# Kernel tuning notes

Hardware: AMD Instinct MI355X
Metric: run time of the kernel (lower is better)

The kernel has to match this reference:

```python
import jax, jax.numpy as jnp
import numpy as np

B, N, C = 128, 512, 512  # batch, num_proposals, hidden_dim
K = 3                    # kernel_size
EPS = 1e-5               # LayerNorm eps (torch default)


def setup_inputs() -> dict:
    key = jax.random.key(0)
    k1, k2, k3, k4 = jax.random.split(key, 4)
    query = jax.random.normal(k1, (B, N, C), dtype=jnp.float32)
    value = jax.random.normal(k2, (B, N, C), dtype=jnp.float32)
    # nn.Linear(C, N+K): store transposed weight [C, N+K] for x @ W
    lim = 1.0 / np.sqrt(C)
    W_lin = jax.random.uniform(k3, (C, N + K), minval=-lim, maxval=lim, dtype=jnp.float32)
    b_lin = jax.random.uniform(k4, (N + K,), minval=-lim, maxval=lim, dtype=jnp.float32)
    gamma = jnp.ones((C,), dtype=jnp.float32)
    beta = jnp.zeros((C,), dtype=jnp.float32)
    return {"query": query, "value": value, "W_lin": W_lin, "b_lin": b_lin,
            "gamma": gamma, "beta": beta}


def reference(query, value, W_lin, b_lin, gamma, beta):
    # dynamic weights: [B, N, N+K]
    dy = jnp.einsum('bnc,ck->bnk', query, W_lin) + b_lin
    dw = dy[..., :K]          # depthwise kernel  [B, N, 3]
    pw = dy[..., K:]          # pointwise weights [B, N(out), N(in)]
    # depthwise conv1d along C, groups=N, padding='same' (cross-correlation)
    vp = jnp.pad(value, ((0, 0), (0, 0), (1, 1)))
    depth = (dw[..., 0:1] * vp[..., 0:C]
             + dw[..., 1:2] * vp[..., 1:C + 1]
             + dw[..., 2:3] * vp[..., 2:C + 2])
    depth = jax.nn.relu(depth)
    # pointwise (1x1) conv across proposals: out[b,m,c] = sum_n pw[b,m,n] * depth[b,n,c]
    out = jnp.einsum('bmn,bnc->bmc', pw, depth)
    # LayerNorm over last dim C
    mu = jnp.mean(out, axis=-1, keepdims=True)
    var = jnp.mean(jnp.square(out - mu), axis=-1, keepdims=True)
    return (out - mu) * jax.lax.rsqrt(var + EPS) * gamma + beta
```

## Files before the change

kernel.cpp:

```cpp
#include <hip/hip_runtime.h>
#include <hip/hip_bf16.h>

typedef unsigned short u16;
typedef unsigned int u32;
typedef __attribute__((ext_vector_type(8))) short short8;
typedef __attribute__((ext_vector_type(8))) unsigned short ushort8;
typedef __attribute__((ext_vector_type(4))) float f32x4;

#define AS1 __attribute__((address_space(1)))
#define AS3 __attribute__((address_space(3)))

#define Bb_ 128
#define Nn_ 512
#define Cc_ 512
#define NK_ 515

__device__ __forceinline__ u16 f2bf(float f) {
    union { float f; u32 i; } t; t.f = f;
    u32 x = t.i;
    u32 r = (x + 0x7fffu + ((x >> 16) & 1u)) >> 16;
    return (u16)r;
}

#define ROWS_PER_WAVE 32
__global__ void prep_kernel(const float* __restrict__ q, const float* __restrict__ W,
                            const float* __restrict__ bl,
                            u16* __restrict__ qbf, float* __restrict__ dw) {
    __shared__ float wc[3][512];
    int tid = threadIdx.x;
    for (int idx = tid; idx < 3 * 512; idx += 256) {
        int j = idx >> 9, c = idx & 511;
        wc[j][c] = W[c * NK_ + j];
    }
    __syncthreads();

    int w = tid >> 6, l = tid & 63;
    int c0 = l * 8;
    float w0[8], w1[8], w2[8];
#pragma unroll
    for (int e = 0; e < 8; e++) {
        w0[e] = wc[0][c0 + e];
        w1[e] = wc[1][c0 + e];
        w2[e] = wc[2][c0 + e];
    }
    float bl0 = bl[0], bl1 = bl[1], bl2 = bl[2];

    size_t row0 = (size_t)blockIdx.x * (4 * ROWS_PER_WAVE) + (size_t)w * ROWS_PER_WAVE;
#pragma unroll 2
    for (int rr = 0; rr < ROWS_PER_WAVE; rr++) {
        size_t row = row0 + rr;
        const float* qr = q + row * Cc_;
        f32x4 x0 = *(const f32x4*)(qr + c0);
        f32x4 x1 = *(const f32x4*)(qr + c0 + 4);
        float xf[8] = {x0[0], x0[1], x0[2], x0[3], x1[0], x1[1], x1[2], x1[3]};
        ushort8 y;
        float s0 = 0.f, s1 = 0.f, s2 = 0.f;
#pragma unroll
        for (int e = 0; e < 8; e++) {
            float qf = xf[e];
            y[e] = f2bf(qf);
            s0 += qf * w0[e];
            s1 += qf * w1[e];
            s2 += qf * w2[e];
        }
        *(ushort8*)(qbf + row * Cc_ + c0) = y;
#pragma unroll
        for (int off = 32; off > 0; off >>= 1) {
            s0 += __shfl_xor(s0, off);
            s1 += __shfl_xor(s1, off);
            s2 += __shfl_xor(s2, off);
        }
        if (l == 0) {
            dw[row * 3 + 0] = s0 + bl0;
            dw[row * 3 + 1] = s1 + bl1;
            dw[row * 3 + 2] = s2 + bl2;
        }
    }
}

__global__ void wt_kernel(const float* __restrict__ W, u16* __restrict__ WT) {
    int n = blockIdx.y;
    int c = blockIdx.x * 256 + threadIdx.x;
    WT[n * Cc_ + c] = f2bf(W[c * NK_ + n + 3]);
}

__global__ void depthT_kernel(const float* __restrict__ val, const float* __restrict__ dw,
                              u16* __restrict__ dT) {
    __shared__ float vt[64][67];
    __shared__ float dws[64][3];
    int b = blockIdx.z;
    int c0 = blockIdx.x * 64;
    int n0 = blockIdx.y * 64;
    int tid = threadIdx.x;

    const float* vbase = val + ((size_t)b * Nn_ + n0) * Cc_;
    for (int idx = tid; idx < 64 * 66; idx += 256) {
        int r = idx / 66, cc = idx % 66;
        int c = c0 - 1 + cc;
        float x = 0.f;
        if (c >= 0 && c < Cc_) x = vbase[(size_t)r * Cc_ + c];
        vt[r][cc] = x;
    }
    if (tid < 192) {
        int r = tid / 3, j = tid % 3;
        dws[r][j] = dw[((size_t)b * Nn_ + n0 + r) * 3 + j];
    }
    __syncthreads();

    int nn = tid & 63;
    int ccb = tid >> 6;
    u16* out = dT + ((size_t)b * Cc_ + c0) * Nn_ + n0;
    float d0 = dws[nn][0], d1 = dws[nn][1], d2 = dws[nn][2];
#pragma unroll
    for (int p = 0; p < 16; p++) {
        int cc = ccb + p * 4;
        float x = d0 * vt[nn][cc] + d1 * vt[nn][cc + 1] + d2 * vt[nn][cc + 2];
        x = x > 0.f ? x : 0.f;
        out[(size_t)cc * Nn_ + nn] = f2bf(x);
    }
}

__global__ __launch_bounds__(256, 2) void gemm1(const u16* __restrict__ A,
                                                const u16* __restrict__ Bt,
                                                u16* __restrict__ Out,
                                                const float* __restrict__ bias) {
    __shared__ __align__(16) u16 lA[2][128 * 32];
    __shared__ __align__(16) u16 lB[2][128 * 32];

    int wg = blockIdx.x;
    int xcd = wg & 7, slot = wg >> 3;
    int b = xcd * 16 + (slot >> 4);
    int tile = slot & 15;
    int tileM = tile >> 2, tileN = tile & 3;

    const u16* Ab = A + ((size_t)b * Nn_ + (size_t)tileM * 128) * Cc_;
    const u16* Bb = Bt + (size_t)tileN * 128 * Cc_;

    int tid = threadIdx.x, w = tid >> 6, l = tid & 63;
    int rsub = l >> 2;
    int csub = l & 3;
    int wm = w & 1, wn = w >> 1;
    int m_off = wm * 64, n_off = wn * 64;
    int row_l = l & 15, quad = l >> 4;

    f32x4 acc[4][4];
#pragma unroll
    for (int i = 0; i < 4; i++)
#pragma unroll
        for (int j = 0; j < 4; j++) acc[i][j] = (f32x4){0.f, 0.f, 0.f, 0.f};

    auto STAGE = [&](int buf, int kt) {
        int kof = kt * 32;
#pragma unroll
        for (int j = 0; j < 2; j++) {
            int seg = w * 2 + j;
            int r = seg * 16 + rsub;
            const u16* gA = Ab + (size_t)r * Cc_ + kof + csub * 8;
            __builtin_amdgcn_global_load_lds((const AS1 u32*)gA,
                                             (AS3 u32*)&lA[buf][seg * 512], 16, 0, 0);
            const u16* gB = Bb + (size_t)r * Cc_ + kof + csub * 8;
            __builtin_amdgcn_global_load_lds((const AS1 u32*)gB,
                                             (AS3 u32*)&lB[buf][seg * 512], 16, 0, 0);
        }
    };

    STAGE(0, 0);
    __syncthreads();
    int cur = 0;
    for (int kt = 0; kt < 16; kt++) {
        if (kt < 15) STAGE(cur ^ 1, kt + 1);

        short8 aF[4], bF[4];
#pragma unroll
        for (int i = 0; i < 4; i++)
            aF[i] = *(const short8*)&lA[cur][(m_off + i * 16 + row_l) * 32 + quad * 8];
#pragma unroll
        for (int j = 0; j < 4; j++)
            bF[j] = *(const short8*)&lB[cur][(n_off + j * 16 + row_l) * 32 + quad * 8];

#pragma unroll
        for (int i = 0; i < 4; i++)
#pragma unroll
            for (int j = 0; j < 4; j++)
                acc[i][j] = __builtin_amdgcn_mfma_f32_16x16x32_bf16(aF[i], bF[j], acc[i][j], 0, 0, 0);

        __syncthreads();
        cur ^= 1;
    }

#pragma unroll
    for (int i = 0; i < 4; i++) {
#pragma unroll
        for (int j = 0; j < 4; j++) {
            int gn = n_off + j * 16 + row_l;
            float bv = bias[tileN * 128 + gn];
#pragma unroll
            for (int r = 0; r < 4; r++) {
                int gm = m_off + i * 16 + quad * 4 + r;
                size_t idx = (size_t)b * Nn_ * Nn_ + (size_t)tileM * 128 * Nn_ +
                             (size_t)tileN * 128 + (size_t)gm * Nn_ + gn;
                Out[idx] = f2bf(acc[i][j][r] + bv);
            }
        }
    }
}

__global__ __launch_bounds__(512, 4) void gemm2_ln(const u16* __restrict__ A,
                                                   const u16* __restrict__ Bt,
                                                   float* __restrict__ out,
                                                   const float* __restrict__ gamma,
                                                   const float* __restrict__ beta) {
    __shared__ __align__(16) u16 lA[2][32 * 32];
    __shared__ __align__(16) u16 lB[2][512 * 32];

    int wg = blockIdx.x;
    int xcd = wg & 7, slot = wg >> 3;
    int b = xcd * 16 + (slot >> 4);
    int tm = slot & 15;

    const u16* Ab = A + ((size_t)b * Nn_ + (size_t)tm * 32) * Nn_;
    const u16* Bb = Bt + (size_t)b * Cc_ * Nn_;

    int tid = threadIdx.x, w = tid >> 6, l = tid & 63;
    int rsub = l >> 2, csub = l & 3;
    int row_l = l & 15, quad = l >> 4;
    int n_off = w * 64;

    f32x4 acc[2][4];
#pragma unroll
    for (int i = 0; i < 2; i++)
#pragma unroll
        for (int j = 0; j < 4; j++) acc[i][j] = (f32x4){0.f, 0.f, 0.f, 0.f};

    auto STAGE = [&](int buf, int kt) {
        int kof = kt * 32;
#pragma unroll
        for (int j = 0; j < 4; j++) {
            int seg = w * 4 + j;
            int r = seg * 16 + rsub;
            const u16* gB = Bb + (size_t)r * Nn_ + kof + csub * 8;
            __builtin_amdgcn_global_load_lds((const AS1 u32*)gB,
                                             (AS3 u32*)&lB[buf][seg * 512], 16, 0, 0);
        }
        if (w < 2) {
            int r = w * 16 + rsub;
            const u16* gA = Ab + (size_t)r * Nn_ + kof + csub * 8;
            __builtin_amdgcn_global_load_lds((const AS1 u32*)gA,
                                             (AS3 u32*)&lA[buf][w * 512], 16, 0, 0);
        }
    };

    STAGE(0, 0);
    __syncthreads();
    int cur = 0;
    for (int kt = 0; kt < 16; kt++) {
        if (kt < 15) STAGE(cur ^ 1, kt + 1);

        short8 aF[2], bF[4];
#pragma unroll
        for (int i = 0; i < 2; i++)
            aF[i] = *(const short8*)&lA[cur][(i * 16 + row_l) * 32 + quad * 8];
#pragma unroll
        for (int j = 0; j < 4; j++)
            bF[j] = *(const short8*)&lB[cur][(n_off + j * 16 + row_l) * 32 + quad * 8];

#pragma unroll
        for (int i = 0; i < 2; i++)
#pragma unroll
            for (int j = 0; j < 4; j++)
                acc[i][j] = __builtin_amdgcn_mfma_f32_16x16x32_bf16(aF[i], bF[j], acc[i][j], 0, 0, 0);

        __syncthreads();
        cur ^= 1;
    }

    float* red  = (float*)&lA[0][0];
    float* musd = (float*)&lB[0][0];

#pragma unroll
    for (int i = 0; i < 2; i++) {
#pragma unroll
        for (int r = 0; r < 4; r++) {
            float a0 = acc[i][0][r], a1 = acc[i][1][r], a2 = acc[i][2][r], a3 = acc[i][3][r];
            float s  = a0 + a1 + a2 + a3;
            float ss = a0 * a0 + a1 * a1 + a2 * a2 + a3 * a3;
#pragma unroll
            for (int off = 8; off > 0; off >>= 1) {
                s  += __shfl_xor(s, off);
                ss += __shfl_xor(ss, off);
            }
            if (row_l == 0) {
                int row = i * 16 + quad * 4 + r;
                red[(w * 32 + row) * 2 + 0] = s;
                red[(w * 32 + row) * 2 + 1] = ss;
            }
        }
    }
    __syncthreads();
    if (w == 0 && l < 32) {
        float s = 0.f, ss = 0.f;
#pragma unroll
        for (int ww = 0; ww < 8; ww++) {
            s  += red[(ww * 32 + l) * 2 + 0];
            ss += red[(ww * 32 + l) * 2 + 1];
        }
        float mu = s * (1.f / 512.f);
        float var = ss * (1.f / 512.f) - mu * mu;
        musd[l] = mu;
        musd[32 + l] = rsqrtf(var + 1e-5f);
    }
    __syncthreads();

    float* outb = out + ((size_t)b * Nn_ + (size_t)tm * 32) * Cc_;
    int gc0 = n_off + row_l;
    float gv[4], bv[4];
#pragma unroll
    for (int j = 0; j < 4; j++) {
        gv[j] = gamma[gc0 + j * 16];
        bv[j] = beta[gc0 + j * 16];
    }
#pragma unroll
    for (int i = 0; i < 2; i++) {
#pragma unroll
        for (int r = 0; r < 4; r++) {
            int row = i * 16 + quad * 4 + r;
            float mu = musd[row], rs = musd[32 + row];
#pragma unroll
            for (int j = 0; j < 4; j++)
                outb[(size_t)row * Cc_ + gc0 + j * 16] = (acc[i][j][r] - mu) * rs * gv[j] + bv[j];
        }
    }
}

extern "C" void kernel_launch(void* const* d_in, const int* in_sizes, int n_in,
                              void* d_out, int out_size, void* d_ws, size_t ws_size,
                              hipStream_t stream) {
    const float* q     = (const float*)d_in[0];
    const float* v     = (const float*)d_in[1];
    const float* W     = (const float*)d_in[2];
    const float* bl    = (const float*)d_in[3];
    const float* gamma = (const float*)d_in[4];
    const float* beta  = (const float*)d_in[5];

    char* ws = (char*)d_ws;
    u16*   WT  = (u16*)ws;
    float* dw  = (float*)(ws + 524288);
    u16*   pw  = (u16*)(ws + 1310720);
    u16*   dT  = (u16*)(ws + 68419584);
    float* out = (float*)d_out;
    u16*   qbf = (u16*)d_out;

    prep_kernel<<<dim3((Bb_ * Nn_) / (4 * ROWS_PER_WAVE)), 256, 0, stream>>>(q, W, bl, qbf, dw);
    wt_kernel<<<dim3(2, 512), 256, 0, stream>>>(W, WT);
    depthT_kernel<<<dim3(8, 8, Bb_), 256, 0, stream>>>(v, dw, dT);

    gemm1<<<dim3(2048), 256, 0, stream>>>(qbf, WT, pw, bl + 3);
    gemm2_ln<<<dim3(2048), 512, 0, stream>>>(pw, dT, out, gamma, beta);
}
```

Baseline: 553.2 us.

## Unify both GEMMs into one templated 128x512 tile kernel

Replaces the two separate GEMM kernels with one templated kernel that computes a 128-row by 512-column output tile per 512-thread workgroup, with each wave holding 8x4 MFMA accumulators. Both GEMMs now launch 512 larger workgroups instead of 2048 smaller ones, so each staged B tile is reused across more rows and A-tile reloads drop. The LayerNorm variant reduces over 128 rows per block. The cost is much higher register pressure (128 accumulator floats per lane), more LDS per block, and fewer workgroups, which may hurt occupancy and latency hiding.

```diff
diff --git a/kernel.cpp b/kernel.cpp
--- a/kernel.cpp
+++ b/kernel.cpp
@@ -120,47 +120,51 @@
     }
 }
 
-__global__ __launch_bounds__(256, 2) void gemm1(const u16* __restrict__ A,
-                                                const u16* __restrict__ Bt,
-                                                u16* __restrict__ Out,
-                                                const float* __restrict__ bias) {
+template <int LN>
+__global__ __launch_bounds__(512, 2) void gemm_k(const u16* __restrict__ A,
+                                                 const u16* __restrict__ Bt,
+                                                 void* __restrict__ Outv,
+                                                 const float* __restrict__ bias,
+                                                 const float* __restrict__ gamma,
+                                                 const float* __restrict__ beta,
+                                                 long strideB) {
     __shared__ __align__(16) u16 lA[2][128 * 32];
-    __shared__ __align__(16) u16 lB[2][128 * 32];
+    __shared__ __align__(16) u16 lB[2][512 * 32];
 
     int wg = blockIdx.x;
     int xcd = wg & 7, slot = wg >> 3;
-    int b = xcd * 16 + (slot >> 4);
-    int tile = slot & 15;
-    int tileM = tile >> 2, tileN = tile & 3;
-
-    const u16* Ab = A + ((size_t)b * Nn_ + (size_t)tileM * 128) * Cc_;
-    const u16* Bb = Bt + (size_t)tileN * 128 * Cc_;
+    int b = xcd * 16 + (slot >> 2);
+    int tm = slot & 3;
+
+    const u16* Ab = A + ((size_t)b * Nn_ + (size_t)tm * 128) * 512;
+    const u16* Bb = Bt + (size_t)b * strideB;
 
     int tid = threadIdx.x, w = tid >> 6, l = tid & 63;
-    int rsub = l >> 2;
-    int csub = l & 3;
-    int wm = w & 1, wn = w >> 1;
-    int m_off = wm * 64, n_off = wn * 64;
+    int rsub = l >> 2, csub = l & 3;
     int row_l = l & 15, quad = l >> 4;
-
-    f32x4 acc[4][4];
-#pragma unroll
-    for (int i = 0; i < 4; i++)
+    int n_off = w * 64;
+
+    f32x4 acc[8][4];
+#pragma unroll
+    for (int i = 0; i < 8; i++)
 #pragma unroll
         for (int j = 0; j < 4; j++) acc[i][j] = (f32x4){0.f, 0.f, 0.f, 0.f};
 
     auto STAGE = [&](int buf, int kt) {
         int kof = kt * 32;
 #pragma unroll
-        for (int j = 0; j < 2; j++) {
-            int seg = w * 2 + j;
+        for (int j = 0; j < 4; j++) {
+            int seg = w * 4 + j;
             int r = seg * 16 + rsub;
-            const u16* gA = Ab + (size_t)r * Cc_ + kof + csub * 8;
-            __builtin_amdgcn_global_load_lds((const AS1 u32*)gA,
-                                             (AS3 u32*)&lA[buf][seg * 512], 16, 0, 0);
-            const u16* gB = Bb + (size_t)r * Cc_ + kof + csub * 8;
+            const u16* gB = Bb + (size_t)r * 512 + kof + csub * 8;
             __builtin_amdgcn_global_load_lds((const AS1 u32*)gB,
                                              (AS3 u32*)&lB[buf][seg * 512], 16, 0, 0);
+        }
+        {
+            int r = w * 16 + rsub;
+            const u16* gA = Ab + (size_t)r * 512 + kof + csub * 8;
+            __builtin_amdgcn_global_load_lds((const AS1 u32*)gA,
+                                             (AS3 u32*)&lA[buf][w * 512], 16, 0, 0);
         }
     };
 
@@ -170,16 +174,16 @@
     for (int kt = 0; kt < 16; kt++) {
         if (kt < 15) STAGE(cur ^ 1, kt + 1);
 
-        short8 aF[4], bF[4];
-#pragma unroll
-        for (int i = 0; i < 4; i++)
-            aF[i] = *(const short8*)&lA[cur][(m_off + i * 16 + row_l) * 32 + quad * 8];
+        short8 aF[8], bF[4];
+#pragma unroll
+        for (int i = 0; i < 8; i++)
+            aF[i] = *(const short8*)&lA[cur][(i * 16 + row_l) * 32 + quad * 8];
 #pragma unroll
         for (int j = 0; j < 4; j++)
             bF[j] = *(const short8*)&lB[cur][(n_off + j * 16 + row_l) * 32 + quad * 8];
 
 #pragma unroll
-        for (int i = 0; i < 4; i++)
+        for (int i = 0; i < 8; i++)
 #pragma unroll
             for (int j = 0; j < 4; j++)
                 acc[i][j] = __builtin_amdgcn_mfma_f32_16x16x32_bf16(aF[i], bF[j], acc[i][j], 0, 0, 0);
@@ -188,146 +192,77 @@
         cur ^= 1;
     }
 
-#pragma unroll
-    for (int i = 0; i < 4; i++) {
+    if (!LN) {
+        u16* outb = (u16*)Outv + ((size_t)b * Nn_ + (size_t)tm * 128) * 512;
 #pragma unroll
         for (int j = 0; j < 4; j++) {
             int gn = n_off + j * 16 + row_l;
-            float bv = bias[tileN * 128 + gn];
+            float bv = bias[gn];
+#pragma unroll
+            for (int i = 0; i < 8; i++) {
+#pragma unroll
+                for (int r = 0; r < 4; r++) {
+                    int gm = i * 16 + quad * 4 + r;
+                    outb[(size_t)gm * 512 + gn] = f2bf(acc[i][j][r] + bv);
+                }
+            }
+        }
+    } else {
+        float* red  = (float*)&lA[0][0];
+        float* musd = (float*)&lB[0][0];
+
+#pragma unroll
+        for (int i = 0; i < 8; i++) {
 #pragma unroll
             for (int r = 0; r < 4; r++) {
-                int gm = m_off + i * 16 + quad * 4 + r;
-                size_t idx = (size_t)b * Nn_ * Nn_ + (size_t)tileM * 128 * Nn_ +
-                             (size_t)tileN * 128 + (size_t)gm * Nn_ + gn;
-                Out[idx] = f2bf(acc[i][j][r] + bv);
-            }
-        }
-    }
-}
-
-__global__ __launch_bounds__(512, 4) void gemm2_ln(const u16* __restrict__ A,
-                                                   const u16* __restrict__ Bt,
-                                                   float* __restrict__ out,
-                                                   const float* __restrict__ gamma,
-                                                   const float* __restrict__ beta) {
-    __shared__ __align__(16) u16 lA[2][32 * 32];
-    __shared__ __align__(16) u16 lB[2][512 * 32];
-
-    int wg = blockIdx.x;
-    int xcd = wg & 7, slot = wg >> 3;
-    int b = xcd * 16 + (slot >> 4);
-    int tm = slot & 15;
-
-    const u16* Ab = A + ((size_t)b * Nn_ + (size_t)tm * 32) * Nn_;
-    const u16* Bb = Bt + (size_t)b * Cc_ * Nn_;
-
-    int tid = threadIdx.x, w = tid >> 6, l = tid & 63;
-    int rsub = l >> 2, csub = l & 3;
-    int row_l = l & 15, quad = l >> 4;
-    int n_off = w * 64;
-
-    f32x4 acc[2][4];
-#pragma unroll
-    for (int i = 0; i < 2; i++)
-#pragma unroll
-        for (int j = 0; j < 4; j++) acc[i][j] = (f32x4){0.f, 0.f, 0.f, 0.f};
-
-    auto STAGE = [&](int buf, int kt) {
-        int kof = kt * 32;
+                float a0 = acc[i][0][r], a1 = acc[i][1][r], a2 = acc[i][2][r], a3 = acc[i][3][r];
+                float s  = a0 + a1 + a2 + a3;
+                float ss = a0 * a0 + a1 * a1 + a2 * a2 + a3 * a3;
+#pragma unroll
+                for (int off = 8; off > 0; off >>= 1) {
+                    s  += __shfl_xor(s, off);
+                    ss += __shfl_xor(ss, off);
+                }
+                if (row_l == 0) {
+                    int row = i * 16 + quad * 4 + r;
+                    red[(w * 128 + row) * 2 + 0] = s;
+                    red[(w * 128 + row) * 2 + 1] = ss;
+                }
+            }
+        }
+        __syncthreads();
+        if (tid < 128) {
+            float s = 0.f, ss = 0.f;
+#pragma unroll
+            for (int ww = 0; ww < 8; ww++) {
+                s  += red[(ww * 128 + tid) * 2 + 0];
+                ss += red[(ww * 128 + tid) * 2 + 1];
+            }
+            float mu = s * (1.f / 512.f);
+            float var = ss * (1.f / 512.f) - mu * mu;
+            musd[tid] = mu;
+            musd[128 + tid] = rsqrtf(var + 1e-5f);
+        }
+        __syncthreads();
+
+        float* outb = (float*)Outv + ((size_t)b * Nn_ + (size_t)tm * 128) * 512;
+        int gc0 = n_off + row_l;
+        float gv[4], bv[4];
 #pragma unroll
         for (int j = 0; j < 4; j++) {
-            int seg = w * 4 + j;
-            int r = seg * 16 + rsub;
-            const u16* gB = Bb + (size_t)r * Nn_ + kof + csub * 8;
-            __builtin_amdgcn_global_load_lds((const AS1 u32*)gB,
-                                             (AS3 u32*)&lB[buf][seg * 512], 16, 0, 0);
-        }
-        if (w < 2) {
-            int r = w * 16 + rsub;
-            const u16* gA = Ab + (size_t)r * Nn_ + kof + csub * 8;
-            __builtin_amdgcn_global_load_lds((const AS1 u32*)gA,
-                                             (AS3 u32*)&lA[buf][w * 512], 16, 0, 0);
-        }
-    };
-
-    STAGE(0, 0);
-    __syncthreads();
-    int cur = 0;
-    for (int kt = 0; kt < 16; kt++) {
-        if (kt < 15) STAGE(cur ^ 1, kt + 1);
-
-        short8 aF[2], bF[4];
-#pragma unroll
-        for (int i = 0; i < 2; i++)
-            aF[i] = *(const short8*)&lA[cur][(i * 16 + row_l) * 32 + quad * 8];
-#pragma unroll
-        for (int j = 0; j < 4; j++)
-            bF[j] = *(const short8*)&lB[cur][(n_off + j * 16 + row_l) * 32 + quad * 8];
-
-#pragma unroll
-        for (int i = 0; i < 2; i++)
-#pragma unroll
-            for (int j = 0; j < 4; j++)
-                acc[i][j] = __builtin_amdgcn_mfma_f32_16x16x32_bf16(aF[i], bF[j], acc[i][j], 0, 0, 0);
-
-        __syncthreads();
-        cur ^= 1;
-    }
-
-    float* red  = (float*)&lA[0][0];
-    float* musd = (float*)&lB[0][0];
-
-#pragma unroll
-    for (int i = 0; i < 2; i++) {
-#pragma unroll
-        for (int r = 0; r < 4; r++) {
-            float a0 = acc[i][0][r], a1 = acc[i][1][r], a2 = acc[i][2][r], a3 = acc[i][3][r];
-            float s  = a0 + a1 + a2 + a3;
-            float ss = a0 * a0 + a1 * a1 + a2 * a2 + a3 * a3;
-#pragma unroll
-            for (int off = 8; off > 0; off >>= 1) {
-                s  += __shfl_xor(s, off);
-                ss += __shfl_xor(ss, off);
-            }
-            if (row_l == 0) {
+            gv[j] = gamma[gc0 + j * 16];
+            bv[j] = beta[gc0 + j * 16];
+        }
+#pragma unroll
+        for (int i = 0; i < 8; i++) {
+#pragma unroll
+            for (int r = 0; r < 4; r++) {
                 int row = i * 16 + quad * 4 + r;
-                red[(w * 32 + row) * 2 + 0] = s;
-                red[(w * 32 + row) * 2 + 1] = ss;
-            }
-        }
-    }
-    __syncthreads();
-    if (w == 0 && l < 32) {
-        float s = 0.f, ss = 0.f;
-#pragma unroll
-        for (int ww = 0; ww < 8; ww++) {
-            s  += red[(ww * 32 + l) * 2 + 0];
-            ss += red[(ww * 32 + l) * 2 + 1];
-        }
-        float mu = s * (1.f / 512.f);
-        float var = ss * (1.f / 512.f) - mu * mu;
-        musd[l] = mu;
-        musd[32 + l] = rsqrtf(var + 1e-5f);
-    }
-    __syncthreads();
-
-    float* outb = out + ((size_t)b * Nn_ + (size_t)tm * 32) * Cc_;
-    int gc0 = n_off + row_l;
-    float gv[4], bv[4];
-#pragma unroll
-    for (int j = 0; j < 4; j++) {
-        gv[j] = gamma[gc0 + j * 16];
-        bv[j] = beta[gc0 + j * 16];
-    }
-#pragma unroll
-    for (int i = 0; i < 2; i++) {
-#pragma unroll
-        for (int r = 0; r < 4; r++) {
-            int row = i * 16 + quad * 4 + r;
-            float mu = musd[row], rs = musd[32 + row];
-#pragma unroll
-            for (int j = 0; j < 4; j++)
-                outb[(size_t)row * Cc_ + gc0 + j * 16] = (acc[i][j][r] - mu) * rs * gv[j] + bv[j];
+                float mu = musd[row], rs = musd[128 + row];
+#pragma unroll
+                for (int j = 0; j < 4; j++)
+                    outb[(size_t)row * 512 + gc0 + j * 16] = (acc[i][j][r] - mu) * rs * gv[j] + bv[j];
+            }
         }
     }
 }
@@ -354,6 +289,7 @@
     wt_kernel<<<dim3(2, 512), 256, 0, stream>>>(W, WT);
     depthT_kernel<<<dim3(8, 8, Bb_), 256, 0, stream>>>(v, dw, dT);
 
-    gemm1<<<dim3(2048), 256, 0, stream>>>(qbf, WT, pw, bl + 3);
-    gemm2_ln<<<dim3(2048), 512, 0, stream>>>(pw, dT, out, gamma, beta);
-}
+    gemm_k<0><<<dim3(512), 512, 0, stream>>>(qbf, WT, pw, bl + 3, nullptr, nullptr, 0L);
+    gemm_k<1><<<dim3(512), 512, 0, stream>>>(pw, dT, out, nullptr, gamma, beta,
+                                             (long)Cc_ * Nn_);
+}
```

After: 513.9 us. 7.1% less time.
